# Optimization experiments

Hardware: AMD Instinct MI355X
Metric: run time of the kernel (lower is better)

Reference implementation:

```python
import jax, jax.numpy as jnp
import numpy as np

PAD = 7                 # init padding
T = 2 * PAD + 1         # T_side_dense = 15 shifts per axis
LAMDA = 1.0             # init lamda
EPS = 1e-16             # hardcoded epsilon in the torch loss body


def _joint_hist(x_out, x_tf_out):
    # Equivalent of F.conv2d(x_out.permute(1,0,2,3), weight=x_tf_out.permute(1,0,2,3), padding=PAD)
    # expressed as T*T shifted matmuls (correlation / cost-volume form).
    bn, k, h, w = x_out.shape
    A = jnp.transpose(x_out, (1, 0, 2, 3))      # (k, bn, h, w)  conv "input"
    B = jnp.transpose(x_tf_out, (1, 0, 2, 3))   # (k, bn, h, w)  conv "weight"
    A_pad = jnp.pad(A, ((0, 0), (0, 0), (PAD, PAD), (PAD, PAD)))

    def step(carry, s):
        dy, dx = s // T, s % T
        sl = jax.lax.dynamic_slice(A_pad, (0, 0, dy, dx), (k, bn, h, w))
        # p[n, o] at this shift = sum_{c,y,x} A_pad[n,c,y+dy,x+dx] * B[o,c,y,x]
        return carry, jnp.einsum('nchw,ochw->no', sl, B)

    _, p = jax.lax.scan(step, None, jnp.arange(T * T))
    # (T*T, k, k) -> (T, T, k, k); matches torch p_i_j.permute(2, 3, 0, 1)
    return p.reshape(T, T, k, k)


def reference(x_out, x_tf_out):
    p = _joint_hist(x_out, x_tf_out)
    # shift to positive; min is detached in torch -> stop_gradient
    p = p - jax.lax.stop_gradient(p.min()) + EPS
    # normalize per shift over the (k, k) joint
    p = p / p.sum(axis=(2, 3), keepdims=True)
    # symmetrize
    p = (p + jnp.swapaxes(p, 2, 3)) / 2.0
    p_i = p.sum(axis=2, keepdims=True)   # (T, T, 1, k) marginal (broadcasts like repeat)
    p_j = p.sum(axis=3, keepdims=True)   # (T, T, k, 1) marginal
    loss = (-p * (jnp.log(p + EPS)
                  - LAMDA * jnp.log(p_i + EPS)
                  - LAMDA * jnp.log(p_j + EPS))).sum() / (T * T)
    return loss


def setup_inputs() -> dict:
    key = jax.random.key(0)
    k1, k2 = jax.random.split(key)
    bn, k, h, w = 16, 10, 224, 224
    # simplex over axis=1 is asserted by the torch module -> use softmax
    x_out = jax.nn.softmax(jax.random.normal(k1, (bn, k, h, w), dtype=jnp.float32), axis=1)
    x_tf_out = jax.nn.softmax(jax.random.normal(k2, (bn, k, h, w), dtype=jnp.float32), axis=1)
    return {"x_out": x_out, "x_tf_out": x_tf_out}
```

## Files before the change

kernel.cpp:

```cpp
#include <hip/hip_runtime.h>
#include <stdint.h>
#include <math.h>


#define PADV 7
#define TS 15
#define KCLS 10
#define HH 224
#define WW 224
#define MD 160
#define NCELL (MD*MD)
#define NBLK 512
#define TY 7
#define AROW 240
#define BSTRIDE 232
#define BPH 240
#define LEPS 1e-16

typedef __attribute__((ext_vector_type(4))) float f32x4;
typedef __attribute__((ext_vector_type(8))) short bf16x8;

__device__ __forceinline__ unsigned short f2bf(float f) {
  union { float f; uint32_t u; } v; v.f = f;
  return (unsigned short)((v.u + 0x7FFFu + ((v.u >> 16) & 1u)) >> 16);
}

__device__ __forceinline__ void glds16(const unsigned short* g, unsigned short* l) {
  __builtin_amdgcn_global_load_lds(
      (const __attribute__((address_space(1))) unsigned int*)g,
      (__attribute__((address_space(3))) unsigned int*)l, 16, 0, 0);
}

__global__ __launch_bounds__(256)
void prep_b(const float* __restrict__ xt, unsigned short* __restrict__ bp) {
  const int idx   = blockIdx.x * 256 + threadIdx.x;
  const int rowid = idx / 29;
  const int chunk = idx - rowid * 29;
  const int x0    = chunk * 8;
  const int yy    = rowid % BPH;
  const int cls   = rowid / BPH;
  const int row   = yy - PADV;
  union { unsigned short h[8]; uint4 v; } out;
  if (row >= 0 && row < HH && x0 < WW) {
    const float* src = xt + ((size_t)cls * HH + row) * WW + x0;
#pragma unroll
    for (int j = 0; j < 8; ++j) out.h[j] = f2bf(src[j]);
  } else {
    out.v = make_uint4(0u, 0u, 0u, 0u);
  }
  *(uint4*)(bp + (size_t)rowid * BSTRIDE + x0) = out.v;
}

__global__ __launch_bounds__(256, 2)
void corr_gemm(const float* __restrict__ xo, const unsigned short* __restrict__ bpad,
               float* __restrict__ partials) {
  __shared__ __align__(16) unsigned short ldsA[KCLS * AROW];
  __shared__ __align__(16) unsigned short ldsB[KCLS * 16 * BSTRIDE];

  const int tid  = threadIdx.x;
  const int bid  = blockIdx.x;
  const int b    = bid >> 5;
  const int y0   = (bid & 31) * TY;

  const int lane = tid & 63;
  const int wv   = tid >> 6;
  const int wm   = wv & 1;
  const int wn   = wv >> 1;
  const int quad = lane >> 4;
  const int l15  = lane & 15;

  f32x4 acc[5][5];
#pragma unroll
  for (int i = 0; i < 5; ++i)
#pragma unroll
    for (int j = 0; j < 5; ++j) acc[i][j] = (f32x4){0.f, 0.f, 0.f, 0.f};

  const float* Ab = xo + (size_t)b * KCLS * HH * WW;
  const unsigned short* Bb = bpad + (size_t)b * KCLS * BPH * BSTRIDE;

  for (int pr = wv; pr < 15 * KCLS; pr += 4) {
    const int r15  = pr / KCLS;
    const int o    = pr - r15 * KCLS;
    const int yy   = y0 + r15;
    const int slot = (y0 - PADV + r15) & 15;
    if (lane < 29)
      glds16(Bb + ((size_t)o * BPH + yy) * BSTRIDE + lane * 8,
             ldsB + (o * 16 + slot) * BSTRIDE);
  }

#pragma unroll
  for (int r = 0; r < 10; ++r) {
    const int t = tid + r * 256;
    if (t < KCLS * AROW) {
      const int n = t / AROW;
      const int i = t - n * AROW;
      const int x = i - PADV;
      float v = 0.f;
      if (x >= 0 && x < WW) v = Ab[((size_t)n * HH + y0) * WW + x];
      ldsA[t] = f2bf(v);
    }
  }
  __syncthreads();

  float va[10];
  for (int y = y0; y < y0 + TY; ++y) {
    const bool more = (y + 1 < y0 + TY);

    if (more) {
      const int yy   = y + 8 + PADV;
      const int slot = (y + 8) & 15;
      for (int ro = wv; ro < KCLS; ro += 4) {
        if (lane < 29)
          glds16(Bb + ((size_t)ro * BPH + yy) * BSTRIDE + lane * 8,
                 ldsB + (ro * 16 + slot) * BSTRIDE);
      }
      const int yl = y + 1;
#pragma unroll
      for (int r = 0; r < 10; ++r) {
        const int t = tid + r * 256;
        float v = 0.f;
        if (t < KCLS * AROW) {
          const int n = t / AROW;
          const int i = t - n * AROW;
          const int x = i - PADV;
          if (x >= 0 && x < WW) v = Ab[((size_t)n * HH + yl) * WW + x];
        }
        va[r] = v;
      }
    }

#pragma unroll 1
    for (int xc = 0; xc < 7; ++xc) {
      const int x0 = xc * 32;
      bf16x8 afrag[5], bfrag[5];
      const int e0 = x0 + quad * 8 + l15;
      const int q  = e0 >> 1;
      const int sh = (e0 & 1) << 4;
#pragma unroll
      for (int mi = 0; mi < 5; ++mi) {
        const int tm = wm * 5 + mi;
        const uint32_t* pa = (const uint32_t*)ldsA + tm * (AROW / 2);
        uint32_t w0 = pa[q], w1 = pa[q + 1], w2 = pa[q + 2],
                 w3 = pa[q + 3], w4 = pa[q + 4];
        union { uint32_t u[4]; bf16x8 v; } cv;
        cv.u[0] = __builtin_amdgcn_alignbit(w1, w0, sh);
        cv.u[1] = __builtin_amdgcn_alignbit(w2, w1, sh);
        cv.u[2] = __builtin_amdgcn_alignbit(w3, w2, sh);
        cv.u[3] = __builtin_amdgcn_alignbit(w4, w3, sh);
        afrag[mi] = cv.v;
      }
      const int slot = (y + PADV - l15) & 15;
#pragma unroll
      for (int ni = 0; ni < 5; ++ni) {
        const int to = wn * 5 + ni;
        bfrag[ni] = *(const bf16x8*)(ldsB + (to * 16 + slot) * BSTRIDE + x0 + quad * 8);
      }
#pragma unroll
      for (int mi = 0; mi < 5; ++mi)
#pragma unroll
        for (int ni = 0; ni < 5; ++ni)
          acc[mi][ni] = __builtin_amdgcn_mfma_f32_16x16x32_bf16(
              afrag[mi], bfrag[ni], acc[mi][ni], 0, 0, 0);
    }

    if (more) {
      __syncthreads();
#pragma unroll
      for (int r = 0; r < 10; ++r) {
        const int t = tid + r * 256;
        if (t < KCLS * AROW) ldsA[t] = f2bf(va[r]);
      }
      __syncthreads();
    }
  }

  float* outp = partials + (size_t)bid * NCELL;
#pragma unroll
  for (int mi = 0; mi < 5; ++mi)
#pragma unroll
    for (int ni = 0; ni < 5; ++ni) {
      const int mrow = (wm * 5 + mi) * 16 + quad * 4;
      const int ncol = (wn * 5 + ni) * 16 + l15;
#pragma unroll
      for (int r = 0; r < 4; ++r)
        outp[(size_t)(mrow + r) * MD + ncol] = acc[mi][ni][r];
    }
}

__global__ __launch_bounds__(256)
void reduce_stage1(const float* __restrict__ partials, float* __restrict__ stage2) {
  const int c  = (blockIdx.x % 100) * 256 + threadIdx.x;
  const int pg = blockIdx.x / 100;
  const float* base = partials + (size_t)pg * 64 * NCELL + c;
  float s0 = 0.f, s1 = 0.f, s2 = 0.f, s3 = 0.f;
  for (int p = 0; p < 64; p += 4) {
    s0 += base[(size_t)(p + 0) * NCELL];
    s1 += base[(size_t)(p + 1) * NCELL];
    s2 += base[(size_t)(p + 2) * NCELL];
    s3 += base[(size_t)(p + 3) * NCELL];
  }
  stage2[(size_t)pg * NCELL + c] = (s0 + s1) + (s2 + s3);
}

__global__ __launch_bounds__(256)
void reduce_final(const float* __restrict__ stage2, float* __restrict__ Cout,
                  float* __restrict__ mins, float* __restrict__ dout) {
  const int c = blockIdx.x * 256 + threadIdx.x;
  if (blockIdx.x == 0 && threadIdx.x == 0) dout[0] = 0.f;
  double s = 0.0;
#pragma unroll
  for (int pg = 0; pg < 8; ++pg) s += (double)stage2[(size_t)pg * NCELL + c];
  const float sf = (float)s;
  Cout[c] = sf;
  const int m  = c / MD;
  const int nn = c - m * MD;
  const bool valid = ((m & 15) < TS) && ((nn & 15) < TS);
  __shared__ float red[256];
  red[threadIdx.x] = valid ? sf : 3.4e38f;
  __syncthreads();
  for (int st = 128; st > 0; st >>= 1) {
    if (threadIdx.x < st)
      red[threadIdx.x] = fminf(red[threadIdx.x], red[threadIdx.x + st]);
    __syncthreads();
  }
  if (threadIdx.x == 0) mins[blockIdx.x] = red[0];
}

__global__ __launch_bounds__(128)
void loss_kernel(const float* __restrict__ Cmat, const float* __restrict__ mins,
                 float* __restrict__ dout) {
  const int s   = blockIdx.x;
  const int dy  = s / TS;
  const int dx  = s - dy * TS;
  const int tid = threadIdx.x;
  __shared__ float fm[128];
  __shared__ double q[100];
  __shared__ double sym[100];
  __shared__ double pi[10], pj[10];
  __shared__ double red[128];

  fm[tid] = (tid < 100) ? mins[tid] : 3.4e38f;
  __syncthreads();
  for (int st = 64; st > 0; st >>= 1) {
    if (tid < st) fm[tid] = fminf(fm[tid], fm[tid + st]);
    __syncthreads();
  }
  const double minv = (double)fm[0];
  __syncthreads();

  if (tid < 100) {
    const int n = tid / 10, o = tid - (tid / 10) * 10;
    const double v = (double)Cmat[(size_t)(n * 16 + dx) * MD + (o * 16 + dy)];
    q[tid] = v - minv + LEPS;
  }
  __syncthreads();
  red[tid] = (tid < 100) ? q[tid] : 0.0;
  __syncthreads();
  for (int st = 64; st > 0; st >>= 1) {
    if (tid < st) red[tid] += red[tid + st];
    __syncthreads();
  }
  const double Z = red[0];
  __syncthreads();
  if (tid < 100) {
    const int n = tid / 10, o = tid - (tid / 10) * 10;
    sym[tid] = (q[n * 10 + o] + q[o * 10 + n]) * 0.5 / Z;
  }
  __syncthreads();
  if (tid < 10) {
    double a = 0.0, bsum = 0.0;
    for (int n2 = 0; n2 < 10; ++n2) {
      a    += sym[n2 * 10 + tid];
      bsum += sym[tid * 10 + n2];
    }
    pi[tid] = a;
    pj[tid] = bsum;
  }
  __syncthreads();
  double term = 0.0;
  if (tid < 100) {
    const int n = tid / 10, o = tid - (tid / 10) * 10;
    const double sp = sym[tid];
    term = -sp * (log(sp + LEPS) - log(pi[o] + LEPS) - log(pj[n] + LEPS));
  }
  red[tid] = term;
  __syncthreads();
  for (int st = 64; st > 0; st >>= 1) {
    if (tid < st) red[tid] += red[tid + st];
    __syncthreads();
  }
  if (tid == 0) atomicAdd(dout, (float)(red[0] / (double)(TS * TS)));
}

extern "C" void kernel_launch(void* const* d_in, const int* in_sizes, int n_in,
                              void* d_out, int out_size, void* d_ws, size_t ws_size,
                              hipStream_t stream) {
  const float* xo = (const float*)d_in[0];
  const float* xt = (const float*)d_in[1];
  float* ws       = (float*)d_ws;

  float* partials = ws;
  float* stage2   = partials + (size_t)NBLK * NCELL;
  float* Cmat     = stage2 + (size_t)8 * NCELL;
  float* mins     = Cmat + NCELL;
  unsigned short* bpad = (unsigned short*)(mins + 128);
  float* out      = (float*)d_out;

  hipLaunchKernelGGL(prep_b,        dim3(4350), dim3(256), 0, stream, xt, bpad);
  hipLaunchKernelGGL(corr_gemm,     dim3(NBLK), dim3(256), 0, stream, xo, bpad, partials);
  hipLaunchKernelGGL(reduce_stage1, dim3(800),  dim3(256), 0, stream, partials, stage2);
  hipLaunchKernelGGL(reduce_final,  dim3(100),  dim3(256), 0, stream, stage2, Cmat, mins, out);
  hipLaunchKernelGGL(loss_kernel,   dim3(225),  dim3(128), 0, stream, Cmat, mins, out);
}
```

Measured before the change: 155.2 us.

## Keep B fragments in registers with DPP row shifts; preload all A rows with pre-shifted copy

The correlation GEMM no longer stages B rows in LDS. Each lane holds its B fragment in registers, and each output row step shifts the fragment across lanes with a DPP row-shift, pulling one new row in from global. All seven A rows are loaded into LDS up front, together with a copy pre-shifted by one element, so fragments are read directly without alignbit work and the per-row syncthreads go away. The stage-one reduction is also vectorised to float4 with a quarter as many blocks. The risks are higher register pressure from the bq, bnext and binj arrays, more LDS per block, and extra global loads of B rows at each x-chunk boundary.

```diff
diff --git a/kernel.cpp b/kernel.cpp
--- a/kernel.cpp
+++ b/kernel.cpp
@@ -12,7 +12,6 @@
 #define NCELL (MD*MD)
 #define NBLK 512
 #define TY 7
-#define AROW 240
 #define BSTRIDE 232
 #define BPH 240
 #define LEPS 1e-16
@@ -23,12 +22,6 @@
 __device__ __forceinline__ unsigned short f2bf(float f) {
   union { float f; uint32_t u; } v; v.f = f;
   return (unsigned short)((v.u + 0x7FFFu + ((v.u >> 16) & 1u)) >> 16);
-}
-
-__device__ __forceinline__ void glds16(const unsigned short* g, unsigned short* l) {
-  __builtin_amdgcn_global_load_lds(
-      (const __attribute__((address_space(1))) unsigned int*)g,
-      (__attribute__((address_space(3))) unsigned int*)l, 16, 0, 0);
 }
 
 __global__ __launch_bounds__(256)
@@ -54,8 +47,7 @@
 __global__ __launch_bounds__(256, 2)
 void corr_gemm(const float* __restrict__ xo, const unsigned short* __restrict__ bpad,
                float* __restrict__ partials) {
-  __shared__ __align__(16) unsigned short ldsA[KCLS * AROW];
-  __shared__ __align__(16) unsigned short ldsB[KCLS * 16 * BSTRIDE];
+  __shared__ __align__(16) unsigned short ldsA[TY * KCLS * 480];
 
   const int tid  = threadIdx.x;
   const int bid  = blockIdx.x;
@@ -76,101 +68,125 @@
     for (int j = 0; j < 5; ++j) acc[i][j] = (f32x4){0.f, 0.f, 0.f, 0.f};
 
   const float* Ab = xo + (size_t)b * KCLS * HH * WW;
-  const unsigned short* Bb = bpad + (size_t)b * KCLS * BPH * BSTRIDE;
-
-  for (int pr = wv; pr < 15 * KCLS; pr += 4) {
-    const int r15  = pr / KCLS;
-    const int o    = pr - r15 * KCLS;
-    const int yy   = y0 + r15;
-    const int slot = (y0 - PADV + r15) & 15;
-    if (lane < 29)
-      glds16(Bb + ((size_t)o * BPH + yy) * BSTRIDE + lane * 8,
-             ldsB + (o * 16 + slot) * BSTRIDE);
-  }
-
-#pragma unroll
-  for (int r = 0; r < 10; ++r) {
-    const int t = tid + r * 256;
-    if (t < KCLS * AROW) {
-      const int n = t / AROW;
-      const int i = t - n * AROW;
-      const int x = i - PADV;
-      float v = 0.f;
-      if (x >= 0 && x < WW) v = Ab[((size_t)n * HH + y0) * WW + x];
-      ldsA[t] = f2bf(v);
-    }
-  }
-  __syncthreads();
-
-  float va[10];
-  for (int y = y0; y < y0 + TY; ++y) {
-    const bool more = (y + 1 < y0 + TY);
-
-    if (more) {
-      const int yy   = y + 8 + PADV;
-      const int slot = (y + 8) & 15;
-      for (int ro = wv; ro < KCLS; ro += 4) {
-        if (lane < 29)
-          glds16(Bb + ((size_t)ro * BPH + yy) * BSTRIDE + lane * 8,
-                 ldsB + (ro * 16 + slot) * BSTRIDE);
+
+  uint32_t bq[5][4], bnext[5][4], binj[5][4];
+#pragma unroll
+  for (int ni = 0; ni < 5; ++ni)
+#pragma unroll
+    for (int r = 0; r < 4; ++r) { bnext[ni][r] = 0; binj[ni][r] = 0; }
+
+  {
+    int yy = y0 + 14 - l15;
+    if (yy < 0) yy = 0;
+#pragma unroll
+    for (int ni = 0; ni < 5; ++ni) {
+      const int cls = b * KCLS + wn * 5 + ni;
+      const unsigned short* p = bpad + ((size_t)cls * BPH + yy) * BSTRIDE + quad * 8;
+      *(uint4*)&bnext[ni][0] = *(const uint4*)p;
+    }
+  }
+
+  for (int t = tid; t < TY * KCLS * 16; t += 256) {
+    const int rc = t >> 4;
+    const int j  = t & 15;
+    const int i  = (j < 7) ? j : (224 + j);
+    ldsA[rc * 480 + i] = 0;
+  }
+  for (int t = tid; t < TY * KCLS * 224; t += 256) {
+    const int rc = t / 224;
+    const int x  = t - rc * 224;
+    const int ry = rc / KCLS;
+    const int cl = rc - ry * KCLS;
+    ldsA[rc * 480 + x + 7] =
+        f2bf(Ab[((size_t)cl * HH + (y0 + ry)) * WW + x]);
+  }
+  __syncthreads();
+  {
+    uint32_t* pw = (uint32_t*)ldsA;
+    for (int t = tid; t < TY * KCLS * 30; t += 256) {
+      const int rc = t / 30;
+      const int ch = t - rc * 30;
+      const uint32_t* src = pw + rc * 240 + ch * 4;
+      uint32_t u0 = src[0], u1 = src[1], u2 = src[2], u3 = src[3];
+      uint32_t u4 = (ch < 29) ? src[4] : 0u;
+      union { uint32_t u[4]; uint4 v; } o;
+      o.u[0] = __builtin_amdgcn_alignbit(u1, u0, 16);
+      o.u[1] = __builtin_amdgcn_alignbit(u2, u1, 16);
+      o.u[2] = __builtin_amdgcn_alignbit(u3, u2, 16);
+      o.u[3] = __builtin_amdgcn_alignbit(u4, u3, 16);
+      *(uint4*)(pw + rc * 240 + 120 + ch * 4) = o.v;
+    }
+  }
+  __syncthreads();
+
+  const uint32_t* lw = (const uint32_t*)ldsA;
+
+#pragma unroll 1
+  for (int xc = 0; xc < 7; ++xc) {
+    const int x0 = xc * 32;
+#pragma unroll
+    for (int ni = 0; ni < 5; ++ni)
+#pragma unroll
+      for (int r = 0; r < 4; ++r) bq[ni][r] = bnext[ni][r];
+
+    const int e0   = x0 + quad * 8 + l15;
+    const int c    = e0 & 1;
+    const int wofs = c * 120 + ((e0 - c) >> 1);
+
+#pragma unroll 1
+    for (int iy = 0; iy < TY; ++iy) {
+      if (iy < TY - 1) {
+        if (l15 == 0) {
+          const int yy = y0 + iy + 15;
+#pragma unroll
+          for (int ni = 0; ni < 5; ++ni) {
+            const int cls = b * KCLS + wn * 5 + ni;
+            const unsigned short* p =
+                bpad + ((size_t)cls * BPH + yy) * BSTRIDE + x0 + quad * 8;
+            *(uint4*)&binj[ni][0] = *(const uint4*)p;
+          }
+        }
+      } else if (xc < 6) {
+        int yy = y0 + 14 - l15;
+        if (yy < 0) yy = 0;
+#pragma unroll
+        for (int ni = 0; ni < 5; ++ni) {
+          const int cls = b * KCLS + wn * 5 + ni;
+          const unsigned short* p =
+              bpad + ((size_t)cls * BPH + yy) * BSTRIDE + (x0 + 32) + quad * 8;
+          *(uint4*)&bnext[ni][0] = *(const uint4*)p;
+        }
       }
-      const int yl = y + 1;
-#pragma unroll
-      for (int r = 0; r < 10; ++r) {
-        const int t = tid + r * 256;
-        float v = 0.f;
-        if (t < KCLS * AROW) {
-          const int n = t / AROW;
-          const int i = t - n * AROW;
-          const int x = i - PADV;
-          if (x >= 0 && x < WW) v = Ab[((size_t)n * HH + yl) * WW + x];
-        }
-        va[r] = v;
-      }
-    }
-
-#pragma unroll 1
-    for (int xc = 0; xc < 7; ++xc) {
-      const int x0 = xc * 32;
-      bf16x8 afrag[5], bfrag[5];
-      const int e0 = x0 + quad * 8 + l15;
-      const int q  = e0 >> 1;
-      const int sh = (e0 & 1) << 4;
+
+      bf16x8 afrag[5];
 #pragma unroll
       for (int mi = 0; mi < 5; ++mi) {
         const int tm = wm * 5 + mi;
-        const uint32_t* pa = (const uint32_t*)ldsA + tm * (AROW / 2);
-        uint32_t w0 = pa[q], w1 = pa[q + 1], w2 = pa[q + 2],
-                 w3 = pa[q + 3], w4 = pa[q + 4];
+        const uint32_t* pa = lw + (iy * KCLS + tm) * 240 + wofs;
         union { uint32_t u[4]; bf16x8 v; } cv;
-        cv.u[0] = __builtin_amdgcn_alignbit(w1, w0, sh);
-        cv.u[1] = __builtin_amdgcn_alignbit(w2, w1, sh);
-        cv.u[2] = __builtin_amdgcn_alignbit(w3, w2, sh);
-        cv.u[3] = __builtin_amdgcn_alignbit(w4, w3, sh);
+        cv.u[0] = pa[0]; cv.u[1] = pa[1]; cv.u[2] = pa[2]; cv.u[3] = pa[3];
         afrag[mi] = cv.v;
       }
-      const int slot = (y + PADV - l15) & 15;
-#pragma unroll
-      for (int ni = 0; ni < 5; ++ni) {
-        const int to = wn * 5 + ni;
-        bfrag[ni] = *(const bf16x8*)(ldsB + (to * 16 + slot) * BSTRIDE + x0 + quad * 8);
+
+#pragma unroll
+      for (int mi = 0; mi < 5; ++mi)
+#pragma unroll
+        for (int ni = 0; ni < 5; ++ni) {
+          union { uint32_t u[4]; bf16x8 v; } bv;
+          bv.u[0] = bq[ni][0]; bv.u[1] = bq[ni][1];
+          bv.u[2] = bq[ni][2]; bv.u[3] = bq[ni][3];
+          acc[mi][ni] = __builtin_amdgcn_mfma_f32_16x16x32_bf16(
+              afrag[mi], bv.v, acc[mi][ni], 0, 0, 0);
+        }
+
+      if (iy < TY - 1) {
+#pragma unroll
+        for (int ni = 0; ni < 5; ++ni)
+#pragma unroll
+          for (int r = 0; r < 4; ++r)
+            bq[ni][r] = (uint32_t)__builtin_amdgcn_update_dpp(
+                (int)binj[ni][r], (int)bq[ni][r], 0x111, 0xF, 0xF, false);
       }
-#pragma unroll
-      for (int mi = 0; mi < 5; ++mi)
-#pragma unroll
-        for (int ni = 0; ni < 5; ++ni)
-          acc[mi][ni] = __builtin_amdgcn_mfma_f32_16x16x32_bf16(
-              afrag[mi], bfrag[ni], acc[mi][ni], 0, 0, 0);
-    }
-
-    if (more) {
-      __syncthreads();
-#pragma unroll
-      for (int r = 0; r < 10; ++r) {
-        const int t = tid + r * 256;
-        if (t < KCLS * AROW) ldsA[t] = f2bf(va[r]);
-      }
-      __syncthreads();
     }
   }
 
@@ -189,17 +205,27 @@
 
 __global__ __launch_bounds__(256)
 void reduce_stage1(const float* __restrict__ partials, float* __restrict__ stage2) {
-  const int c  = (blockIdx.x % 100) * 256 + threadIdx.x;
-  const int pg = blockIdx.x / 100;
-  const float* base = partials + (size_t)pg * 64 * NCELL + c;
-  float s0 = 0.f, s1 = 0.f, s2 = 0.f, s3 = 0.f;
+  const int pg = blockIdx.x / 25;
+  const int cg = blockIdx.x - pg * 25;
+  const int cb = cg * 1024 + threadIdx.x * 4;
+  const float* base = partials + (size_t)pg * 64 * NCELL + cb;
+  float4 s0 = {0,0,0,0}, s1 = {0,0,0,0}, s2 = {0,0,0,0}, s3 = {0,0,0,0};
   for (int p = 0; p < 64; p += 4) {
-    s0 += base[(size_t)(p + 0) * NCELL];
-    s1 += base[(size_t)(p + 1) * NCELL];
-    s2 += base[(size_t)(p + 2) * NCELL];
-    s3 += base[(size_t)(p + 3) * NCELL];
-  }
-  stage2[(size_t)pg * NCELL + c] = (s0 + s1) + (s2 + s3);
+    float4 a = *(const float4*)(base + (size_t)(p + 0) * NCELL);
+    float4 bb = *(const float4*)(base + (size_t)(p + 1) * NCELL);
+    float4 cc = *(const float4*)(base + (size_t)(p + 2) * NCELL);
+    float4 d = *(const float4*)(base + (size_t)(p + 3) * NCELL);
+    s0.x += a.x; s0.y += a.y; s0.z += a.z; s0.w += a.w;
+    s1.x += bb.x; s1.y += bb.y; s1.z += bb.z; s1.w += bb.w;
+    s2.x += cc.x; s2.y += cc.y; s2.z += cc.z; s2.w += cc.w;
+    s3.x += d.x; s3.y += d.y; s3.z += d.z; s3.w += d.w;
+  }
+  float4 o;
+  o.x = (s0.x + s1.x) + (s2.x + s3.x);
+  o.y = (s0.y + s1.y) + (s2.y + s3.y);
+  o.z = (s0.z + s1.z) + (s2.z + s3.z);
+  o.w = (s0.w + s1.w) + (s2.w + s3.w);
+  *(float4*)(stage2 + (size_t)pg * NCELL + cb) = o;
 }
 
 __global__ __launch_bounds__(256)
@@ -308,7 +334,7 @@
 
   hipLaunchKernelGGL(prep_b,        dim3(4350), dim3(256), 0, stream, xt, bpad);
   hipLaunchKernelGGL(corr_gemm,     dim3(NBLK), dim3(256), 0, stream, xo, bpad, partials);
-  hipLaunchKernelGGL(reduce_stage1, dim3(800),  dim3(256), 0, stream, partials, stage2);
+  hipLaunchKernelGGL(reduce_stage1, dim3(200),  dim3(256), 0, stream, partials, stage2);
   hipLaunchKernelGGL(reduce_final,  dim3(100),  dim3(256), 0, stream, stage2, Cmat, mins, out);
   hipLaunchKernelGGL(loss_kernel,   dim3(225),  dim3(128), 0, stream, Cmat, mins, out);
 }
```

After: 172.9 us. 1.11x slower.

## Pre-pad A to bf16 and stream A fragments from global into registers

Applied to the files above, without the earlier changes.

The prep kernel now also converts x_out into a padded, packed bf16 buffer. The correlation GEMM then drops its LDS A tile and loads each wave's A fragments directly from global memory into registers, double-buffered one x-chunk ahead, with a single barrier per row instead of two. The two-stage partial reduction is merged into one 100-block kernel that sums all 512 partials in double, removing a launch and an intermediate buffer but giving much less parallelism for the reduction.

```diff
diff --git a/kernel.cpp b/kernel.cpp
--- a/kernel.cpp
+++ b/kernel.cpp
@@ -12,9 +12,9 @@
 #define NCELL (MD*MD)
 #define NBLK 512
 #define TY 7
-#define AROW 240
 #define BSTRIDE 232
 #define BPH 240
+#define ADW 120
 #define LEPS 1e-16
 
 typedef __attribute__((ext_vector_type(4))) float f32x4;
@@ -31,30 +31,60 @@
       (__attribute__((address_space(3))) unsigned int*)l, 16, 0, 0);
 }
 
+struct U5 { uint32_t u[5]; };
+
+__device__ __forceinline__ void ldA5(const uint32_t* p, U5& d) {
+  uint4 t;
+  __builtin_memcpy(&t, p, 16);
+  d.u[0] = t.x; d.u[1] = t.y; d.u[2] = t.z; d.u[3] = t.w;
+  d.u[4] = p[4];
+}
+
+#define BPREP_BLOCKS 4350
+#define APREP_BLOCKS 4200
 __global__ __launch_bounds__(256)
-void prep_b(const float* __restrict__ xt, unsigned short* __restrict__ bp) {
-  const int idx   = blockIdx.x * 256 + threadIdx.x;
-  const int rowid = idx / 29;
-  const int chunk = idx - rowid * 29;
-  const int x0    = chunk * 8;
-  const int yy    = rowid % BPH;
-  const int cls   = rowid / BPH;
-  const int row   = yy - PADV;
-  union { unsigned short h[8]; uint4 v; } out;
-  if (row >= 0 && row < HH && x0 < WW) {
-    const float* src = xt + ((size_t)cls * HH + row) * WW + x0;
-#pragma unroll
-    for (int j = 0; j < 8; ++j) out.h[j] = f2bf(src[j]);
+void prep(const float* __restrict__ xo, const float* __restrict__ xt,
+          unsigned short* __restrict__ bp, uint32_t* __restrict__ ap) {
+  if (blockIdx.x < BPREP_BLOCKS) {
+    const int idx   = blockIdx.x * 256 + threadIdx.x;
+    const int rowid = idx / 29;
+    const int chunk = idx - rowid * 29;
+    const int x0    = chunk * 8;
+    const int yy    = rowid % BPH;
+    const int cls   = rowid / BPH;
+    const int row   = yy - PADV;
+    union { unsigned short h[8]; uint4 v; } out;
+    if (row >= 0 && row < HH && x0 < WW) {
+      const float* src = xt + ((size_t)cls * HH + row) * WW + x0;
+#pragma unroll
+      for (int j = 0; j < 8; ++j) out.h[j] = f2bf(src[j]);
+    } else {
+      out.v = make_uint4(0u, 0u, 0u, 0u);
+    }
+    *(uint4*)(bp + (size_t)rowid * BSTRIDE + x0) = out.v;
   } else {
-    out.v = make_uint4(0u, 0u, 0u, 0u);
-  }
-  *(uint4*)(bp + (size_t)rowid * BSTRIDE + x0) = out.v;
+    const int idx   = (blockIdx.x - BPREP_BLOCKS) * 256 + threadIdx.x;
+    const int rowid = idx / 30;
+    const int wg    = idx - rowid * 30;
+    const float* src = xo + (size_t)rowid * WW;
+    float e[8];
+#pragma unroll
+    for (int j = 0; j < 8; ++j) {
+      const int x = 8 * wg + j - PADV;
+      e[j] = (x >= 0 && x < WW) ? src[x] : 0.f;
+    }
+    union { uint32_t u[4]; uint4 v; } o;
+#pragma unroll
+    for (int k = 0; k < 4; ++k)
+      o.u[k] = (uint32_t)f2bf(e[2 * k]) | ((uint32_t)f2bf(e[2 * k + 1]) << 16);
+    *(uint4*)(ap + (size_t)rowid * ADW + 4 * wg) = o.v;
+  }
 }
 
 __global__ __launch_bounds__(256, 2)
-void corr_gemm(const float* __restrict__ xo, const unsigned short* __restrict__ bpad,
+void corr_gemm(const uint32_t* __restrict__ apad,
+               const unsigned short* __restrict__ bpad,
                float* __restrict__ partials) {
-  __shared__ __align__(16) unsigned short ldsA[KCLS * AROW];
   __shared__ __align__(16) unsigned short ldsB[KCLS * 16 * BSTRIDE];
 
   const int tid  = threadIdx.x;
@@ -69,14 +99,17 @@
   const int quad = lane >> 4;
   const int l15  = lane & 15;
 
+  const int shA    = (l15 & 1) << 4;
+  const int laneWd = quad * 4 + (l15 >> 1);
+
   f32x4 acc[5][5];
 #pragma unroll
   for (int i = 0; i < 5; ++i)
 #pragma unroll
     for (int j = 0; j < 5; ++j) acc[i][j] = (f32x4){0.f, 0.f, 0.f, 0.f};
 
-  const float* Ab = xo + (size_t)b * KCLS * HH * WW;
   const unsigned short* Bb = bpad + (size_t)b * KCLS * BPH * BSTRIDE;
+  const uint32_t* Abase = apad + ((size_t)(b * KCLS + wm * 5) * HH) * ADW;
 
   for (int pr = wv; pr < 15 * KCLS; pr += 4) {
     const int r15  = pr / KCLS;
@@ -88,25 +121,19 @@
              ldsB + (o * 16 + slot) * BSTRIDE);
   }
 
-#pragma unroll
-  for (int r = 0; r < 10; ++r) {
-    const int t = tid + r * 256;
-    if (t < KCLS * AROW) {
-      const int n = t / AROW;
-      const int i = t - n * AROW;
-      const int x = i - PADV;
-      float v = 0.f;
-      if (x >= 0 && x < WW) v = Ab[((size_t)n * HH + y0) * WW + x];
-      ldsA[t] = f2bf(v);
-    }
-  }
-  __syncthreads();
-
-  float va[10];
-  for (int y = y0; y < y0 + TY; ++y) {
-    const bool more = (y + 1 < y0 + TY);
-
-    if (more) {
+  U5 bufA[5], bufB[5];
+#pragma unroll
+  for (int mi = 0; mi < 5; ++mi)
+    ldA5(Abase + ((size_t)mi * HH + y0) * ADW + laneWd, bufA[mi]);
+
+  __syncthreads();
+
+  auto step = [&](int t, U5 (&use)[5], U5 (&pre)[5]) {
+    const int ydiv = t / 7;
+    const int xc   = t - 7 * ydiv;
+    const int y    = y0 + ydiv;
+
+    if (xc == 0) {
       const int yy   = y + 8 + PADV;
       const int slot = (y + 8) & 15;
       for (int ro = wv; ro < KCLS; ro += 4) {
@@ -114,64 +141,52 @@
           glds16(Bb + ((size_t)ro * BPH + yy) * BSTRIDE + lane * 8,
                  ldsB + (ro * 16 + slot) * BSTRIDE);
       }
-      const int yl = y + 1;
-#pragma unroll
-      for (int r = 0; r < 10; ++r) {
-        const int t = tid + r * 256;
-        float v = 0.f;
-        if (t < KCLS * AROW) {
-          const int n = t / AROW;
-          const int i = t - n * AROW;
-          const int x = i - PADV;
-          if (x >= 0 && x < WW) v = Ab[((size_t)n * HH + yl) * WW + x];
-        }
-        va[r] = v;
-      }
-    }
-
-#pragma unroll 1
-    for (int xc = 0; xc < 7; ++xc) {
-      const int x0 = xc * 32;
-      bf16x8 afrag[5], bfrag[5];
-      const int e0 = x0 + quad * 8 + l15;
-      const int q  = e0 >> 1;
-      const int sh = (e0 & 1) << 4;
-#pragma unroll
-      for (int mi = 0; mi < 5; ++mi) {
-        const int tm = wm * 5 + mi;
-        const uint32_t* pa = (const uint32_t*)ldsA + tm * (AROW / 2);
-        uint32_t w0 = pa[q], w1 = pa[q + 1], w2 = pa[q + 2],
-                 w3 = pa[q + 3], w4 = pa[q + 4];
-        union { uint32_t u[4]; bf16x8 v; } cv;
-        cv.u[0] = __builtin_amdgcn_alignbit(w1, w0, sh);
-        cv.u[1] = __builtin_amdgcn_alignbit(w2, w1, sh);
-        cv.u[2] = __builtin_amdgcn_alignbit(w3, w2, sh);
-        cv.u[3] = __builtin_amdgcn_alignbit(w4, w3, sh);
-        afrag[mi] = cv.v;
-      }
-      const int slot = (y + PADV - l15) & 15;
-#pragma unroll
-      for (int ni = 0; ni < 5; ++ni) {
-        const int to = wn * 5 + ni;
-        bfrag[ni] = *(const bf16x8*)(ldsB + (to * 16 + slot) * BSTRIDE + x0 + quad * 8);
-      }
+    }
+
+    if (t < 48) {
+      const int t1    = t + 1;
+      const int ydiv1 = t1 / 7;
+      const int xc1   = t1 - 7 * ydiv1;
+      const int y1    = y0 + ydiv1;
 #pragma unroll
       for (int mi = 0; mi < 5; ++mi)
-#pragma unroll
-        for (int ni = 0; ni < 5; ++ni)
-          acc[mi][ni] = __builtin_amdgcn_mfma_f32_16x16x32_bf16(
-              afrag[mi], bfrag[ni], acc[mi][ni], 0, 0, 0);
-    }
-
-    if (more) {
-      __syncthreads();
-#pragma unroll
-      for (int r = 0; r < 10; ++r) {
-        const int t = tid + r * 256;
-        if (t < KCLS * AROW) ldsA[t] = f2bf(va[r]);
-      }
-      __syncthreads();
-    }
+        ldA5(Abase + ((size_t)mi * HH + y1) * ADW + xc1 * 16 + laneWd, pre[mi]);
+    }
+
+    bf16x8 afrag[5];
+#pragma unroll
+    for (int mi = 0; mi < 5; ++mi) {
+      union { uint32_t u[4]; bf16x8 v; } cv;
+      cv.u[0] = __builtin_amdgcn_alignbit(use[mi].u[1], use[mi].u[0], shA);
+      cv.u[1] = __builtin_amdgcn_alignbit(use[mi].u[2], use[mi].u[1], shA);
+      cv.u[2] = __builtin_amdgcn_alignbit(use[mi].u[3], use[mi].u[2], shA);
+      cv.u[3] = __builtin_amdgcn_alignbit(use[mi].u[4], use[mi].u[3], shA);
+      afrag[mi] = cv.v;
+    }
+
+    const int x0    = xc * 32;
+    const int slotB = (y + PADV - l15) & 15;
+    bf16x8 bfrag[5];
+#pragma unroll
+    for (int ni = 0; ni < 5; ++ni) {
+      const int to = wn * 5 + ni;
+      bfrag[ni] = *(const bf16x8*)(ldsB + (to * 16 + slotB) * BSTRIDE + x0 + quad * 8);
+    }
+
+#pragma unroll
+    for (int mi = 0; mi < 5; ++mi)
+#pragma unroll
+      for (int ni = 0; ni < 5; ++ni)
+        acc[mi][ni] = __builtin_amdgcn_mfma_f32_16x16x32_bf16(
+            afrag[mi], bfrag[ni], acc[mi][ni], 0, 0, 0);
+
+    if (xc == 6 && t < 48) __syncthreads();
+  };
+
+  for (int ph = 0; ph < 25; ++ph) {
+    const int t0 = 2 * ph;
+    step(t0, bufA, bufB);
+    if (t0 + 1 < 49) step(t0 + 1, bufB, bufA);
   }
 
   float* outp = partials + (size_t)bid * NCELL;
@@ -188,29 +203,19 @@
 }
 
 __global__ __launch_bounds__(256)
-void reduce_stage1(const float* __restrict__ partials, float* __restrict__ stage2) {
-  const int c  = (blockIdx.x % 100) * 256 + threadIdx.x;
-  const int pg = blockIdx.x / 100;
-  const float* base = partials + (size_t)pg * 64 * NCELL + c;
-  float s0 = 0.f, s1 = 0.f, s2 = 0.f, s3 = 0.f;
-  for (int p = 0; p < 64; p += 4) {
-    s0 += base[(size_t)(p + 0) * NCELL];
-    s1 += base[(size_t)(p + 1) * NCELL];
-    s2 += base[(size_t)(p + 2) * NCELL];
-    s3 += base[(size_t)(p + 3) * NCELL];
-  }
-  stage2[(size_t)pg * NCELL + c] = (s0 + s1) + (s2 + s3);
-}
-
-__global__ __launch_bounds__(256)
-void reduce_final(const float* __restrict__ stage2, float* __restrict__ Cout,
-                  float* __restrict__ mins, float* __restrict__ dout) {
+void reduce_all(const float* __restrict__ partials, float* __restrict__ Cout,
+                float* __restrict__ mins, float* __restrict__ dout) {
   const int c = blockIdx.x * 256 + threadIdx.x;
-  if (blockIdx.x == 0 && threadIdx.x == 0) dout[0] = 0.f;
-  double s = 0.0;
-#pragma unroll
-  for (int pg = 0; pg < 8; ++pg) s += (double)stage2[(size_t)pg * NCELL + c];
-  const float sf = (float)s;
+  if (c == 0) dout[0] = 0.f;
+  double s0 = 0.0, s1 = 0.0, s2 = 0.0, s3 = 0.0;
+  const float* base = partials + c;
+  for (int p = 0; p < NBLK; p += 4) {
+    s0 += (double)base[(size_t)(p + 0) * NCELL];
+    s1 += (double)base[(size_t)(p + 1) * NCELL];
+    s2 += (double)base[(size_t)(p + 2) * NCELL];
+    s3 += (double)base[(size_t)(p + 3) * NCELL];
+  }
+  const float sf = (float)((s0 + s1) + (s2 + s3));
   Cout[c] = sf;
   const int m  = c / MD;
   const int nn = c - m * MD;
@@ -300,15 +305,15 @@
   float* ws       = (float*)d_ws;
 
   float* partials = ws;
-  float* stage2   = partials + (size_t)NBLK * NCELL;
-  float* Cmat     = stage2 + (size_t)8 * NCELL;
+  float* Cmat     = partials + (size_t)NBLK * NCELL;
   float* mins     = Cmat + NCELL;
   unsigned short* bpad = (unsigned short*)(mins + 128);
+  uint32_t* apad  = (uint32_t*)(bpad + (size_t)160 * BPH * BSTRIDE);
   float* out      = (float*)d_out;
 
-  hipLaunchKernelGGL(prep_b,        dim3(4350), dim3(256), 0, stream, xt, bpad);
-  hipLaunchKernelGGL(corr_gemm,     dim3(NBLK), dim3(256), 0, stream, xo, bpad, partials);
-  hipLaunchKernelGGL(reduce_stage1, dim3(800),  dim3(256), 0, stream, partials, stage2);
-  hipLaunchKernelGGL(reduce_final,  dim3(100),  dim3(256), 0, stream, stage2, Cmat, mins, out);
-  hipLaunchKernelGGL(loss_kernel,   dim3(225),  dim3(128), 0, stream, Cmat, mins, out);
-}
+  hipLaunchKernelGGL(prep,       dim3(BPREP_BLOCKS + APREP_BLOCKS), dim3(256), 0, stream,
+                     xo, xt, bpad, apad);
+  hipLaunchKernelGGL(corr_gemm,  dim3(NBLK), dim3(256), 0, stream, apad, bpad, partials);
+  hipLaunchKernelGGL(reduce_all, dim3(100),  dim3(256), 0, stream, partials, Cmat, mins, out);
+  hipLaunchKernelGGL(loss_kernel,dim3(225),  dim3(128), 0, stream, Cmat, mins, out);
+}
```

New measurement: 179.1 us. 1.15x slower.
